# Kernel tuning notes

Hardware: AMD Instinct MI355X
Metric: run time of the kernel (lower is better)

## Reference

```python
import jax, jax.numpy as jnp
import numpy as np

OUT = 8          # roi_layer_output
SR = 2           # sampling_ratio per bin edge (fixed; mmcv default-adaptive approximated)
SCALE = 1.0 / 16.0  # 1/featmap_stride


def _xavier(key, fan_out, fan_in):
    std = float(np.sqrt(2.0 / (fan_in + fan_out)))
    return jax.random.normal(key, (fan_out, fan_in), dtype=jnp.float32) * std


def setup_inputs() -> dict:
    key = jax.random.key(0)
    ks = jax.random.split(key, 8)
    B, C, T, H, W = 16, 528, 32, 28, 28
    R = 256
    img = H * 16  # 448, input-image resolution implied by stride 16
    x = jax.random.normal(ks[0], (B, C, T, H, W), dtype=jnp.float32)
    bidx = jax.random.randint(ks[1], (R,), 0, B).astype(jnp.float32)
    xy1 = jax.random.uniform(ks[2], (R, 2), dtype=jnp.float32) * (img * 0.6)
    wh = jax.random.uniform(ks[3], (R, 2), dtype=jnp.float32) * (img * 0.35) + 16.0
    bbox = jnp.concatenate([bidx[:, None], xy1, xy1 + wh], axis=1)  # [R,5] (b,x1,y1,x2,y2)
    w1 = _xavier(ks[4], 128, 528)
    w2 = _xavier(ks[5], 32, 128)
    w3 = _xavier(ks[6], 1, 32)
    return {
        'x': x, 'bbox': bbox,
        'w1': w1, 'b1': jnp.zeros((128,), jnp.float32),
        'w2': w2, 'b2': jnp.zeros((32,), jnp.float32),
        'w3': w3, 'b3': jnp.zeros((1,), jnp.float32),
    }


def roi_align(feat, bbox):
    # feat: [B, C, H, W]; bbox: [R, 5]. Aligned RoIAlign, output [R, C, OUT, OUT].
    B, C, H, W = feat.shape
    bidx = bbox[:, 0].astype(jnp.int32)
    x1 = bbox[:, 1] * SCALE - 0.5
    y1 = bbox[:, 2] * SCALE - 0.5
    x2 = bbox[:, 3] * SCALE - 0.5
    y2 = bbox[:, 4] * SCALE - 0.5
    bin_w = (x2 - x1) / OUT
    bin_h = (y2 - y1) / OUT
    S = OUT * SR
    off = (jnp.arange(S, dtype=jnp.float32) + 0.5) / SR  # sample centers in bin units
    xs = x1[:, None] + off[None, :] * bin_w[:, None]  # [R,S]
    ys = y1[:, None] + off[None, :] * bin_h[:, None]  # [R,S]
    y = ys[:, :, None]  # [R,S,1]
    xg = xs[:, None, :]  # [R,1,S]
    valid = ((y > -1.0) & (y < H) & (xg > -1.0) & (xg < W)).astype(feat.dtype)  # [R,S,S]
    yc = jnp.clip(y, 0.0, H - 1)
    xc = jnp.clip(xg, 0.0, W - 1)
    y0 = jnp.floor(yc).astype(jnp.int32)
    x0 = jnp.floor(xc).astype(jnp.int32)
    y1i = jnp.minimum(y0 + 1, H - 1)
    x1i = jnp.minimum(x0 + 1, W - 1)
    ly = (yc - y0)[..., None]  # [R,S,1,1]
    lx = (xc - x0)[..., None]  # [R,1,S,1]
    hy, hx = 1.0 - ly, 1.0 - lx
    b = bidx[:, None, None]
    # gathers -> [R,S,S,C]
    v00 = feat[b, :, y0, x0]
    v01 = feat[b, :, y0, x1i]
    v10 = feat[b, :, y1i, x0]
    v11 = feat[b, :, y1i, x1i]
    v = hy * hx * v00 + hy * lx * v01 + ly * hx * v10 + ly * lx * v11
    v = v * valid[..., None]
    # average SRxSR samples per bin -> [R,OUT,OUT,C] -> [R,C,OUT,OUT]
    v = v.reshape(-1, OUT, SR, OUT, SR, C).mean(axis=(2, 4))
    return jnp.transpose(v, (0, 3, 1, 2))


def reference(x, bbox, w1, b1, w2, b2, w3, b3):
    # SingleRoIExtractor3D with with_temporal_pool=True: mean over T, then RoIAlign.
    feat = jnp.mean(x, axis=2)                 # [B,C,H,W]
    r = roi_align(feat, bbox)                  # [R,C,8,8]
    # temporal pool is a no-op (t==1); spatial pool -> [R,C]
    r = r.mean(axis=(2, 3))
    h = jax.nn.relu(r @ w1.T + b1)             # dropout is identity at inference
    h = h @ w2.T + b2
    return h @ w3.T + b3                       # [R,1]
```

## Files before the change

kernel.cpp:

```cpp
#include <hip/hip_runtime.h>
#include <hip/hip_bf16.h>

#define BB 16
#define CC 528
#define TT 32
#define HW 784
#define NPIX4 196
#define NOUT4 1655808
#define NJ 128
#define NROI 256
#define CHUNK 48

__global__ __launch_bounds__(256) void tmean_kernel(const float4* __restrict__ x4,
                                                    float4* __restrict__ feat4) {
    int idx = blockIdx.x * 256 + threadIdx.x;
    if (idx >= NOUT4) return;
    int bc = idx / NPIX4;
    int p4 = idx - bc * NPIX4;
    const float4* xp = x4 + (size_t)bc * (TT * NPIX4) + p4;
    float sx = 0.f, sy = 0.f, sz = 0.f, sw = 0.f;
#pragma unroll 8
    for (int t = 0; t < TT; ++t) {
        float4 v = xp[(size_t)t * NPIX4];
        sx += v.x; sy += v.y; sz += v.z; sw += v.w;
    }
    float4 o;
    o.x = sx * 0.03125f; o.y = sy * 0.03125f; o.z = sz * 0.03125f; o.w = sw * 0.03125f;
    feat4[idx] = o;
}

__global__ void transpose_w1(const float* __restrict__ w1, float* __restrict__ w1T) {
    int c = blockIdx.x;
    int j = threadIdx.x;
    w1T[c * NJ + j] = w1[j * CC + c];
}

__global__ __launch_bounds__(256) void proj_kernel(const float* __restrict__ feat,
                                                   const float* __restrict__ w1T,
                                                   float* __restrict__ g) {
    __shared__ float fs[CHUNK * 56];
    __shared__ float w1s[CHUNK * NJ];
    int tile = blockIdx.x;
    int b = blockIdx.y;
    int tid = threadIdx.x;
    int jg = tid & 31;
    int pr = tid >> 5;
    int p0 = tile * 56;
    float acc[4][7];
#pragma unroll
    for (int a = 0; a < 4; ++a)
#pragma unroll
        for (int i = 0; i < 7; ++i) acc[a][i] = 0.f;

    const float* featb = feat + (size_t)b * CC * HW;

    for (int c0 = 0; c0 < CC; c0 += CHUNK) {
        for (int t = tid; t < CHUNK * 56; t += 256) {
            int cl = t / 56;
            int pp = t - cl * 56;
            fs[t] = featb[(size_t)(c0 + cl) * HW + p0 + pp];
        }
        for (int t = tid; t < CHUNK * NJ; t += 256) {
            w1s[t] = w1T[c0 * NJ + t];
        }
        __syncthreads();
#pragma unroll 4
        for (int cl = 0; cl < CHUNK; ++cl) {
            float4 wv = *(const float4*)&w1s[cl * NJ + jg * 4];
            float fv[7];
#pragma unroll
            for (int i = 0; i < 7; ++i) fv[i] = fs[cl * 56 + pr * 7 + i];
#pragma unroll
            for (int i = 0; i < 7; ++i) {
                acc[0][i] += wv.x * fv[i];
                acc[1][i] += wv.y * fv[i];
                acc[2][i] += wv.z * fv[i];
                acc[3][i] += wv.w * fv[i];
            }
        }
        __syncthreads();
    }
#pragma unroll
    for (int i = 0; i < 7; ++i) {
        int p = p0 + pr * 7 + i;
        float4* gp = (float4*)(g + ((size_t)b * HW + p) * NJ + jg * 4);
        float4 o;
        o.x = acc[0][i]; o.y = acc[1][i]; o.z = acc[2][i]; o.w = acc[3][i];
        *gp = o;
    }
}

__global__ __launch_bounds__(256) void roi_mlp_kernel(const float* __restrict__ g,
                                                      const float* __restrict__ bbox,
                                                      const float* __restrict__ b1,
                                                      const float* __restrict__ w2,
                                                      const float* __restrict__ b2,
                                                      const float* __restrict__ w3,
                                                      const float* __restrict__ b3,
                                                      float* __restrict__ out) {
    __shared__ float red[2][NJ];
    __shared__ float h1s[NJ];
    __shared__ float h2s[32];
    __shared__ float w2s[32 * 129];
    int r = blockIdx.x;
    int tid = threadIdx.x;

    for (int t = tid; t < 32 * NJ; t += 256) {
        w2s[(t >> 7) * 129 + (t & 127)] = w2[t];
    }

    int b = (int)bbox[5 * r];
    float x1 = bbox[5 * r + 1] * 0.0625f - 0.5f;
    float y1 = bbox[5 * r + 2] * 0.0625f - 0.5f;
    float x2 = bbox[5 * r + 3] * 0.0625f - 0.5f;
    float y2 = bbox[5 * r + 4] * 0.0625f - 0.5f;
    float bw = (x2 - x1) * 0.125f;
    float bh = (y2 - y1) * 0.125f;

    int j = tid & 127;
    int grp = tid >> 7;
    const float* gb = g + (size_t)b * HW * NJ;
    float acc = 0.f;

    for (int s = grp; s < 256; s += 2) {
        int iy = s >> 4, ix = s & 15;
        float yy = y1 + (iy + 0.5f) * 0.5f * bh;
        float xx = x1 + (ix + 0.5f) * 0.5f * bw;
        if (yy > -1.f && yy < 28.f && xx > -1.f && xx < 28.f) {
            float yc = fminf(fmaxf(yy, 0.f), 27.f);
            float xc = fminf(fmaxf(xx, 0.f), 27.f);
            int y0 = (int)floorf(yc);
            int x0 = (int)floorf(xc);
            int y1i = min(y0 + 1, 27);
            int x1i = min(x0 + 1, 27);
            float ly = yc - (float)y0, lx = xc - (float)x0;
            float hy = 1.f - ly, hx = 1.f - lx;
            const float* r0 = gb + (size_t)(y0 * 28) * NJ;
            const float* r1p = gb + (size_t)(y1i * 28) * NJ;
            float v00 = r0[x0 * NJ + j];
            float v01 = r0[x1i * NJ + j];
            float v10 = r1p[x0 * NJ + j];
            float v11 = r1p[x1i * NJ + j];
            acc += hy * hx * v00 + hy * lx * v01 + ly * hx * v10 + ly * lx * v11;
        }
    }
    red[grp][j] = acc;
    __syncthreads();
    if (tid < NJ) {
        float tot = (red[0][tid] + red[1][tid]) * (1.f / 256.f) + b1[tid];
        h1s[tid] = fmaxf(tot, 0.f);
    }
    __syncthreads();
    if (tid < 32) {
        float a2 = b2[tid];
#pragma unroll 8
        for (int jj = 0; jj < NJ; ++jj) a2 += w2s[tid * 129 + jj] * h1s[jj];
        h2s[tid] = a2;
    }
    __syncthreads();
    if (tid == 0) {
        float o = b3[0];
#pragma unroll
        for (int k = 0; k < 32; ++k) o += w3[k] * h2s[k];
        out[r] = o;
    }
}

extern "C" void kernel_launch(void* const* d_in, const int* in_sizes, int n_in,
                              void* d_out, int out_size, void* d_ws, size_t ws_size,
                              hipStream_t stream) {
    (void)in_sizes; (void)n_in; (void)out_size; (void)ws_size;
    const float* x    = (const float*)d_in[0];
    const float* bbox = (const float*)d_in[1];
    const float* w1   = (const float*)d_in[2];
    const float* b1   = (const float*)d_in[3];
    const float* w2   = (const float*)d_in[4];
    const float* b2   = (const float*)d_in[5];
    const float* w3   = (const float*)d_in[6];
    const float* b3   = (const float*)d_in[7];
    float* out = (float*)d_out;

    float* feat = (float*)d_ws;
    float* g    = feat + (size_t)BB * CC * HW;
    float* w1T  = g + (size_t)BB * HW * NJ;

    tmean_kernel<<<NOUT4 / 256, 256, 0, stream>>>((const float4*)x, (float4*)feat);
    transpose_w1<<<CC, NJ, 0, stream>>>(w1, w1T);
    proj_kernel<<<dim3(14, BB), 256, 0, stream>>>(feat, w1T, g);
    roi_mlp_kernel<<<NROI, 256, 0, stream>>>(g, bbox, b1, w2, b2, w3, b3, out);
}
```

Measured before the change: 1.210 ms.

## Fuse temporal mean into projection kernel with double-buffered register prefetch

Removes the separate temporal-mean kernel and its feature buffer. Each of 448 threads now loads 32 time samples for one channel and pixel straight from the input and sums them into the shared feature tile. The next 8-channel chunk of input and weights is prefetched into registers while the current chunk is computed from double-buffered shared memory. This avoids writing and re-reading the averaged feature map, but it leaves only 224 blocks to stream the whole input and raises per-thread register pressure.

Result: faster. 1.122 ms (-7.3%).

```diff
diff --git a/kernel.cpp b/kernel.cpp
--- a/kernel.cpp
+++ b/kernel.cpp
@@ -5,29 +5,10 @@
 #define CC 528
 #define TT 32
 #define HW 784
-#define NPIX4 196
-#define NOUT4 1655808
 #define NJ 128
 #define NROI 256
-#define CHUNK 48
-
-__global__ __launch_bounds__(256) void tmean_kernel(const float4* __restrict__ x4,
-                                                    float4* __restrict__ feat4) {
-    int idx = blockIdx.x * 256 + threadIdx.x;
-    if (idx >= NOUT4) return;
-    int bc = idx / NPIX4;
-    int p4 = idx - bc * NPIX4;
-    const float4* xp = x4 + (size_t)bc * (TT * NPIX4) + p4;
-    float sx = 0.f, sy = 0.f, sz = 0.f, sw = 0.f;
-#pragma unroll 8
-    for (int t = 0; t < TT; ++t) {
-        float4 v = xp[(size_t)t * NPIX4];
-        sx += v.x; sy += v.y; sz += v.z; sw += v.w;
-    }
-    float4 o;
-    o.x = sx * 0.03125f; o.y = sy * 0.03125f; o.z = sz * 0.03125f; o.w = sw * 0.03125f;
-    feat4[idx] = o;
-}
+#define CL 8
+#define NCHUNK 66
 
 __global__ void transpose_w1(const float* __restrict__ w1, float* __restrict__ w1T) {
     int c = blockIdx.x;
@@ -35,58 +16,87 @@
     w1T[c * NJ + j] = w1[j * CC + c];
 }
 
-__global__ __launch_bounds__(256) void proj_kernel(const float* __restrict__ feat,
-                                                   const float* __restrict__ w1T,
-                                                   float* __restrict__ g) {
-    __shared__ float fs[CHUNK * 56];
-    __shared__ float w1s[CHUNK * NJ];
-    int tile = blockIdx.x;
-    int b = blockIdx.y;
-    int tid = threadIdx.x;
-    int jg = tid & 31;
-    int pr = tid >> 5;
-    int p0 = tile * 56;
-    float acc[4][7];
+__global__ __launch_bounds__(448) void fused_proj_kernel(const float* __restrict__ x,
+                                                         const float* __restrict__ w1T,
+                                                         float* __restrict__ g) {
+    __shared__ __align__(16) float fs[2][CL * 56];
+    __shared__ __align__(16) float w1s[2][CL * NJ];
+    const int tile = blockIdx.x;
+    const int b    = blockIdx.y;
+    const int tid  = threadIdx.x;
+    const int cl   = tid / 56;
+    const int px   = tid - cl * 56;
+    const int p0   = tile * 56;
+    const int jg   = tid & 31;
+    const int pr   = tid >> 5;
+
+    const float* xb = x + ((size_t)b * CC + cl) * (size_t)(TT * HW) + p0 + px;
+
+    float acc[4][4];
 #pragma unroll
     for (int a = 0; a < 4; ++a)
 #pragma unroll
-        for (int i = 0; i < 7; ++i) acc[a][i] = 0.f;
+        for (int i = 0; i < 4; ++i) acc[a][i] = 0.f;
 
-    const float* featb = feat + (size_t)b * CC * HW;
+    float tv[TT];
+#pragma unroll
+    for (int t = 0; t < TT; ++t) tv[t] = xb[t * HW];
+    float wa = w1T[tid];
+    float wb = w1T[448 + tid];
+    float wc = (tid < 128) ? w1T[896 + tid] : 0.f;
+    {
+        float s = 0.f;
+#pragma unroll
+        for (int t = 0; t < TT; ++t) s += tv[t];
+        fs[0][tid] = s * 0.03125f;
+        w1s[0][tid] = wa;
+        w1s[0][448 + tid] = wb;
+        if (tid < 128) w1s[0][896 + tid] = wc;
+    }
+    __syncthreads();
 
-    for (int c0 = 0; c0 < CC; c0 += CHUNK) {
-        for (int t = tid; t < CHUNK * 56; t += 256) {
-            int cl = t / 56;
-            int pp = t - cl * 56;
-            fs[t] = featb[(size_t)(c0 + cl) * HW + p0 + pp];
+    for (int ch = 0; ch < NCHUNK; ++ch) {
+        const int nxt = ch + 1;
+        if (nxt < NCHUNK) {
+            const float* xq = xb + (size_t)nxt * (CL * TT * HW);
+#pragma unroll
+            for (int t = 0; t < TT; ++t) tv[t] = xq[t * HW];
+            const float* wq = w1T + nxt * (CL * NJ);
+            wa = wq[tid];
+            wb = wq[448 + tid];
+            if (tid < 128) wc = wq[896 + tid];
         }
-        for (int t = tid; t < CHUNK * NJ; t += 256) {
-            w1s[t] = w1T[c0 * NJ + t];
+        const float* fsb = fs[ch & 1];
+        const float* wsb = w1s[ch & 1];
+#pragma unroll
+        for (int c = 0; c < CL; ++c) {
+            float4 wv = *(const float4*)&wsb[c * NJ + jg * 4];
+            float4 fv = *(const float4*)&fsb[c * 56 + pr * 4];
+            acc[0][0] += wv.x * fv.x; acc[0][1] += wv.x * fv.y; acc[0][2] += wv.x * fv.z; acc[0][3] += wv.x * fv.w;
+            acc[1][0] += wv.y * fv.x; acc[1][1] += wv.y * fv.y; acc[1][2] += wv.y * fv.z; acc[1][3] += wv.y * fv.w;
+            acc[2][0] += wv.z * fv.x; acc[2][1] += wv.z * fv.y; acc[2][2] += wv.z * fv.z; acc[2][3] += wv.z * fv.w;
+            acc[3][0] += wv.w * fv.x; acc[3][1] += wv.w * fv.y; acc[3][2] += wv.w * fv.z; acc[3][3] += wv.w * fv.w;
         }
-        __syncthreads();
-#pragma unroll 4
-        for (int cl = 0; cl < CHUNK; ++cl) {
-            float4 wv = *(const float4*)&w1s[cl * NJ + jg * 4];
-            float fv[7];
+        if (nxt < NCHUNK) {
+            float s = 0.f;
 #pragma unroll
-            for (int i = 0; i < 7; ++i) fv[i] = fs[cl * 56 + pr * 7 + i];
-#pragma unroll
-            for (int i = 0; i < 7; ++i) {
-                acc[0][i] += wv.x * fv[i];
-                acc[1][i] += wv.y * fv[i];
-                acc[2][i] += wv.z * fv[i];
-                acc[3][i] += wv.w * fv[i];
-            }
+            for (int t = 0; t < TT; ++t) s += tv[t];
+            float* fw = fs[nxt & 1];
+            float* ww = w1s[nxt & 1];
+            fw[tid] = s * 0.03125f;
+            ww[tid] = wa;
+            ww[448 + tid] = wb;
+            if (tid < 128) ww[896 + tid] = wc;
         }
         __syncthreads();
     }
+
+    float* gp = g + ((size_t)(b * HW + p0 + pr * 4)) * NJ + jg * 4;
 #pragma unroll
-    for (int i = 0; i < 7; ++i) {
-        int p = p0 + pr * 7 + i;
-        float4* gp = (float4*)(g + ((size_t)b * HW + p) * NJ + jg * 4);
+    for (int i = 0; i < 4; ++i) {
         float4 o;
         o.x = acc[0][i]; o.y = acc[1][i]; o.z = acc[2][i]; o.w = acc[3][i];
-        *gp = o;
+        *(float4*)(gp + (size_t)i * NJ) = o;
     }
 }
 
@@ -180,12 +190,10 @@
     const float* b3   = (const float*)d_in[7];
     float* out = (float*)d_out;
 
-    float* feat = (float*)d_ws;
-    float* g    = feat + (size_t)BB * CC * HW;
-    float* w1T  = g + (size_t)BB * HW * NJ;
+    float* g   = (float*)d_ws;
+    float* w1T = g + (size_t)BB * HW * NJ;
 
-    tmean_kernel<<<NOUT4 / 256, 256, 0, stream>>>((const float4*)x, (float4*)feat);
     transpose_w1<<<CC, NJ, 0, stream>>>(w1, w1T);
-    proj_kernel<<<dim3(14, BB), 256, 0, stream>>>(feat, w1T, g);
+    fused_proj_kernel<<<dim3(14, BB), 448, 0, stream>>>(x, w1T, g);
     roi_mlp_kernel<<<NROI, 256, 0, stream>>>(g, bbox, b1, w2, b2, w3, b3, out);
 }
```
